# Kernel optimization log

Hardware: AMD Instinct MI355X
Metric: run time of the kernel (lower is better)

Reference implementation:

```python
import jax, jax.numpy as jnp
import numpy as np
import math

B, S, D, K = 8, 2048, 1024, 64
EPS = 1e-5

def _ln(x):
    m = jnp.mean(x, axis=-1, keepdims=True)
    v = jnp.mean((x - m) ** 2, axis=-1, keepdims=True)
    return (x - m) * jax.lax.rsqrt(v + EPS)

def setup_inputs() -> dict:
    key = jax.random.key(0)
    ks = jax.random.split(key, 14)
    s = 0.02
    return {
        "x":  jax.random.normal(ks[0], (B, S, D), dtype=jnp.float32),
        "Wk": jax.random.normal(ks[1], (D, K), dtype=jnp.float32) * s,
        "bk": jnp.zeros((K,), dtype=jnp.float32),
        "Wq": jax.random.normal(ks[2], (D, K), dtype=jnp.float32) * s,
        "bq": jnp.zeros((K,), dtype=jnp.float32),
        "Wv": jax.random.normal(ks[3], (D, D), dtype=jnp.float32) * s,
        "bv": jnp.zeros((D,), dtype=jnp.float32),
        "Wb": jax.random.normal(ks[4], (D, 1), dtype=jnp.float32) * s,
        "bb": jnp.zeros((1,), dtype=jnp.float32),
        "W1": jax.random.normal(ks[5], (D, D), dtype=jnp.float32) * s,
        "b1": jnp.zeros((D,), dtype=jnp.float32),
        "g1": jnp.ones((D,), dtype=jnp.float32),
        "be1": jnp.zeros((D,), dtype=jnp.float32),
    }

def reference(x, Wk, bk, Wq, bq, Wv, bv, Wb, bb, W1, b1, g1, be1):
    scale = 1.0 / math.sqrt(K)
    keys    = (jnp.einsum('bsd,dk->bsk', x, Wk) + bk) * scale   # [B,S,K]
    queries = jnp.einsum('bsd,dk->bsk', x, Wq) + bq             # [B,S,K]
    values  = jnp.einsum('bsd,de->bse', x, Wv) + bv             # [B,S,D]
    biases  = jnp.einsum('bsd,do->bso', x, Wb) + bb             # [B,S,1]
    # scores[b,i,j] = keys[b,i] . queries[b,j] + biases[b,i]
    scores = jax.nn.sigmoid(jnp.einsum('bik,bjk->bij', keys, queries) + biases)
    attention = jnp.einsum('bij,bjd->bid', scores, values)      # [B,S,D]
    res = _ln(x + attention) * g1 + be1
    feedforward = jax.nn.relu(jnp.einsum('bsd,de->bse', res, W1) + b1)
    return _ln(res + feedforward)
```

## Files before the change

### kernel.cpp

```cpp
#include <hip/hip_runtime.h>
#include <math.h>


typedef __bf16 bf16_t;
typedef __bf16 bf16x4_t __attribute__((ext_vector_type(4)));
typedef __bf16 bf16x8_t __attribute__((ext_vector_type(8)));
typedef float  f32x4    __attribute__((ext_vector_type(4)));

#define DEV static __device__ __forceinline__

DEV void gll16(const void* g, void* l) {
  __builtin_amdgcn_global_load_lds(
      (const __attribute__((address_space(1))) void*)g,
      (__attribute__((address_space(3))) void*)l, 16, 0, 0);
}

__global__ __launch_bounds__(512, 4) void vt_kq(
    const bf16_t* __restrict__ Wvt, const bf16_t* __restrict__ x_bf,
    bf16_t* __restrict__ vt, const float* __restrict__ bv,
    const bf16_t* __restrict__ Wkqt, bf16_t* __restrict__ kqO,
    const float* __restrict__ bk, const float* __restrict__ bq) {
  __shared__ bf16_t SM[24576];
  const int tid = threadIdx.x;
  const int wid = tid >> 6, l = tid & 63;
  const int lr = l & 15, lh = l >> 4;
  const int sw = (lh ^ ((lr >> 1) & 3)) * 8;

  if (blockIdx.x < 512) {
#define ASH(s) (&SM[(s) << 13])
#define BSH(s) (&SM[16384 + ((s) << 12)])
    const int nwg = 512;
    const int orig = blockIdx.x;
    const int lid = (orig & 7) * (nwg >> 3) + (orig >> 3);
    const int bx = lid / 4;
    const int by = lid % 4;
    const int m0 = by * 256, n0 = bx * 128;
    const int lda = 1024, ldb = 1024, ldc = 16384;

    const int wr = wid >> 1, wc = wid & 1;
    const int sRow = tid >> 2;
    const int sSl = (tid & 3) ^ ((tid >> 3) & 3);
    const bf16_t* Asrc = Wvt + (long)(m0 + sRow) * lda + sSl * 8;
    const bf16_t* Bsrc = x_bf + (long)(n0 + sRow) * ldb + sSl * 8;
    const long aStep = (long)128 * lda;

    const int aOff = (wr * 64 + lr) * 32 + sw;
    const int bOff = (wc * 64 + lr) * 32 + sw;

    f32x4 acc[4][4] = {};

    gll16(Asrc, ASH(0) + tid * 8);
    gll16(Asrc + aStep, ASH(0) + 4096 + tid * 8);
    gll16(Bsrc, BSH(0) + tid * 8);

    for (int h = 0; h < 32; ++h) {
      const int s = h & 1;
      asm volatile("s_waitcnt vmcnt(0)" ::: "memory");
      __builtin_amdgcn_sched_barrier(0);
      __builtin_amdgcn_s_barrier();
      if (h + 1 < 32) {
        const bf16_t* a_ = Asrc + (h + 1) * 32;
        const bf16_t* b_ = Bsrc + (h + 1) * 32;
        gll16(a_, ASH(s ^ 1) + tid * 8);
        gll16(a_ + aStep, ASH(s ^ 1) + 4096 + tid * 8);
        gll16(b_, BSH(s ^ 1) + tid * 8);
      }
      bf16x8_t aF[4], bF[4];
#pragma unroll
      for (int m = 0; m < 4; ++m) aF[m] = *(const bf16x8_t*)(ASH(s) + aOff + m * 512);
#pragma unroll
      for (int n = 0; n < 4; ++n) bF[n] = *(const bf16x8_t*)(BSH(s) + bOff + n * 512);
      asm volatile("s_waitcnt lgkmcnt(0)" ::: "memory");
      __builtin_amdgcn_sched_barrier(0);
      __builtin_amdgcn_s_setprio(1);
#pragma unroll
      for (int m = 0; m < 4; ++m)
#pragma unroll
        for (int n = 0; n < 4; ++n)
          acc[m][n] = __builtin_amdgcn_mfma_f32_16x16x32_bf16(aF[m], bF[n], acc[m][n], 0, 0, 0);
      __builtin_amdgcn_s_setprio(0);
    }

    const int rowb = m0 + wr * 64 + lh * 4;
    const int colb = n0 + wc * 64 + lr;
#pragma unroll
    for (int m = 0; m < 4; ++m)
#pragma unroll
      for (int n = 0; n < 4; ++n) {
        const f32x4 v = acc[m][n];
        const int cc = colb + n * 16;
#pragma unroll
        for (int r = 0; r < 4; ++r) {
          const int rr = rowb + m * 16 + r;
          vt[(long)rr * ldc + cc] = (bf16_t)(v[r] + bv[rr]);
        }
      }
#undef ASH
#undef BSH
  } else {
#define ASH(s) (&SM[(s) << 12])
#define BSH(s) (&SM[8192 + ((s) << 12)])
    const int m0 = (blockIdx.x - 512) * 128;

    const int sRow = tid >> 2;
    const int sSl = (tid & 3) ^ ((tid >> 3) & 3);
    const bf16_t* Asrc = x_bf + (long)(m0 + sRow) * 1024 + sSl * 8;
    const bf16_t* Bsrc = Wkqt + (long)sRow * 1024 + sSl * 8;

    const int aOff = (wid * 16 + lr) * 32 + sw;

    f32x4 acc[8] = {};

    gll16(Asrc, ASH(0) + tid * 8);
    gll16(Bsrc, BSH(0) + tid * 8);

    for (int h = 0; h < 32; ++h) {
      const int s = h & 1;
      asm volatile("s_waitcnt vmcnt(0)" ::: "memory");
      __builtin_amdgcn_sched_barrier(0);
      __builtin_amdgcn_s_barrier();
      if (h + 1 < 32) {
        gll16(Asrc + (h + 1) * 32, ASH(s ^ 1) + tid * 8);
        gll16(Bsrc + (h + 1) * 32, BSH(s ^ 1) + tid * 8);
      }
      const bf16x8_t aF = *(const bf16x8_t*)(ASH(s) + aOff);
      bf16x8_t bF[8];
#pragma unroll
      for (int j = 0; j < 8; ++j)
        bF[j] = *(const bf16x8_t*)(BSH(s) + (j * 16 + lr) * 32 + sw);
      asm volatile("s_waitcnt lgkmcnt(0)" ::: "memory");
      __builtin_amdgcn_sched_barrier(0);
      __builtin_amdgcn_s_setprio(1);
#pragma unroll
      for (int j = 0; j < 8; ++j)
        acc[j] = __builtin_amdgcn_mfma_f32_16x16x32_bf16(aF, bF[j], acc[j], 0, 0, 0);
      __builtin_amdgcn_s_setprio(0);
    }

    __builtin_amdgcn_s_barrier();
#pragma unroll
    for (int j = 0; j < 8; ++j) {
      const f32x4 v = acc[j];
      const int cl = j * 16 + lr;
      const float b = (cl < 64) ? bk[cl] : bq[cl - 64];
      const float sc = (cl < 64) ? 0.125f : 1.0f;
#pragma unroll
      for (int r = 0; r < 4; ++r) {
        const int rl = wid * 16 + lh * 4 + r;
        SM[rl * 128 + (cl ^ (lh << 4))] = (bf16_t)((v[r] + b) * sc);
      }
    }
    __builtin_amdgcn_s_barrier();
    const int chunk = tid & 15, rsub = tid >> 4;
#pragma unroll
    for (int pp = 0; pp < 4; ++pp) {
      const int rl = pp * 32 + rsub;
      const int sc = chunk ^ (((rl >> 2) & 3) << 1);
      const bf16x8_t vv = *(const bf16x8_t*)&SM[rl * 128 + sc * 8];
      *(bf16x8_t*)&kqO[(long)(m0 + rl) * 128 + chunk * 8] = vv;
    }
#undef ASH
#undef BSH
  }
}

template <int MODE, int MFAST>
__global__ __launch_bounds__(512, 4) void gemm128n(
    const bf16_t* __restrict__ A, const bf16_t* __restrict__ B,
    bf16_t* __restrict__ C, int K, int lda, int ldb, int ldc,
    const float* __restrict__ aux0) {
  const int gx = gridDim.x, gy = gridDim.y;
  const int nwg = gx * gy;
  const int orig = blockIdx.x + gx * blockIdx.y;
  const int lid = (orig & 7) * (nwg >> 3) + (orig >> 3);
  const int bx = MFAST ? (lid / gy) : (lid % gx);
  const int by = MFAST ? (lid % gy) : (lid / gx);
  const int m0 = by * 256, n0 = bx * 128;

  __shared__ bf16_t SM[24576];
#define ASH(s) (&SM[(s) << 13])
#define BSH(s) (&SM[16384 + ((s) << 12)])

  const int tid = threadIdx.x;
  const int wid = tid >> 6, l = tid & 63;
  const int wr = wid >> 1, wc = wid & 1;
  const int lr = l & 15, lh = l >> 4;

  const int sRow = tid >> 2;
  const int sSl = (tid & 3) ^ ((tid >> 3) & 3);
  const bf16_t* Asrc = A + (long)(m0 + sRow) * lda + sSl * 8;
  const bf16_t* Bsrc = B + (long)(n0 + sRow) * ldb + sSl * 8;
  const long aStep = (long)128 * lda;

  const int sw = (lh ^ ((lr >> 1) & 3)) * 8;
  const int aOff = (wr * 64 + lr) * 32 + sw;
  const int bOff = (wc * 64 + lr) * 32 + sw;

  f32x4 acc[4][4] = {};
  const int NT = K >> 5;

  gll16(Asrc, ASH(0) + tid * 8);
  gll16(Asrc + aStep, ASH(0) + 4096 + tid * 8);
  gll16(Bsrc, BSH(0) + tid * 8);

  for (int h = 0; h < NT; ++h) {
    const int s = h & 1;
    asm volatile("s_waitcnt vmcnt(0)" ::: "memory");
    __builtin_amdgcn_sched_barrier(0);
    __builtin_amdgcn_s_barrier();
    if (h + 1 < NT) {
      const bf16_t* a_ = Asrc + (h + 1) * 32;
      const bf16_t* b_ = Bsrc + (h + 1) * 32;
      gll16(a_, ASH(s ^ 1) + tid * 8);
      gll16(a_ + aStep, ASH(s ^ 1) + 4096 + tid * 8);
      gll16(b_, BSH(s ^ 1) + tid * 8);
    }
    bf16x8_t aF[4], bF[4];
#pragma unroll
    for (int m = 0; m < 4; ++m) aF[m] = *(const bf16x8_t*)(ASH(s) + aOff + m * 512);
#pragma unroll
    for (int n = 0; n < 4; ++n) bF[n] = *(const bf16x8_t*)(BSH(s) + bOff + n * 512);
    asm volatile("s_waitcnt lgkmcnt(0)" ::: "memory");
    __builtin_amdgcn_sched_barrier(0);
    __builtin_amdgcn_s_setprio(1);
#pragma unroll
    for (int m = 0; m < 4; ++m)
#pragma unroll
      for (int n = 0; n < 4; ++n)
        acc[m][n] = __builtin_amdgcn_mfma_f32_16x16x32_bf16(aF[m], bF[n], acc[m][n], 0, 0, 0);
    __builtin_amdgcn_s_setprio(0);
  }

  const int rowb = m0 + wr * 64 + lh * 4;
  const int colb = n0 + wc * 64 + lr;
#pragma unroll
  for (int m = 0; m < 4; ++m)
#pragma unroll
    for (int n = 0; n < 4; ++n) {
      const f32x4 v = acc[m][n];
      const int cc = colb + n * 16;
#pragma unroll
      for (int r = 0; r < 4; ++r) {
        const int rr = rowb + m * 16 + r;
        const float val = v[r];
        if constexpr (MODE == 1) {
          C[(long)rr * ldc + cc] = (bf16_t)(val + aux0[rr]);
        } else {
          C[(long)rr * ldc + cc] = (bf16_t)fmaxf(val + aux0[cc], 0.0f);
        }
      }
    }
#undef ASH
#undef BSH
}

template <int MODE>
__global__ __launch_bounds__(512, 2) void gemm256p(
    const bf16_t* __restrict__ A, const bf16_t* __restrict__ B,
    bf16_t* __restrict__ C, int K, int lda, int ldb, int ldc,
    long sAb, long sBb, long sCb, const float* __restrict__ aux0) {
  const int gx = gridDim.x, gy = gridDim.y;
  const int gxy = gx * gy;
  const int nwg = gxy * (int)gridDim.z;
  const int orig = blockIdx.x + gx * blockIdx.y + gxy * blockIdx.z;
  const int lid = (orig & 7) * (nwg >> 3) + (orig >> 3);
  const int bz = lid / gxy;
  const int rem = lid - bz * gxy;
  const int bx = rem % gx;
  const int by = rem / gx;

  A += (long)bz * sAb;
  B += (long)bz * sBb;
  const int m0 = by * 256, n0 = bx * 256;

  __shared__ bf16_t SM[65536];
#define ASH(b, h) (&SM[(((b)*2 + (h)) << 13)])
#define BSH(b, h) (&SM[32768 + (((b)*2 + (h)) << 13)])

  const int tid = threadIdx.x;
  const int wid = tid >> 6, l = tid & 63;
  const int wr = wid >> 2, wc = wid & 3;
  const int lr = l & 15, lh = l >> 4;

  const int sRow = tid >> 2;
  const int sSl = (tid & 3) ^ ((tid >> 3) & 3);
  const bf16_t* Asrc = A + (long)(m0 + sRow) * lda + sSl * 8;
  const bf16_t* Bsrc = B + (long)(n0 + sRow) * ldb + sSl * 8;
  const long aStep = (long)128 * lda, bStep = (long)128 * ldb;

#define STAGE_A(b, h, kt) do { \
    const bf16_t* s_ = Asrc + (kt) * 64 + (h) * 32; \
    gll16(s_,         ASH(b, h) + tid * 8); \
    gll16(s_ + aStep, ASH(b, h) + 4096 + tid * 8); } while (0)
#define STAGE_B(b, h, kt) do { \
    const bf16_t* s_ = Bsrc + (kt) * 64 + (h) * 32; \
    gll16(s_,         BSH(b, h) + tid * 8); \
    gll16(s_ + bStep, BSH(b, h) + 4096 + tid * 8); } while (0)

  const int sw = (lh ^ ((lr >> 1) & 3)) * 8;
  const int aOff = (wr * 128 + lr) * 32 + sw;
  const int bOff = (wc * 64 + lr) * 32 + sw;

  f32x4 acc[8][4] = {};
  const int NT = K >> 6;

#define LGKM(n) do { \
    asm volatile("s_waitcnt lgkmcnt(" #n ")" ::: "memory"); \
    __builtin_amdgcn_sched_barrier(0); } while (0)
#define MFMA16(AS, BS, mo) do { \
    __builtin_amdgcn_s_setprio(1); \
    _Pragma("unroll") for (int m = 0; m < 4; ++m) \
    _Pragma("unroll") for (int n = 0; n < 4; ++n) \
      acc[m + (mo)][n] = __builtin_amdgcn_mfma_f32_16x16x32_bf16(AS[m], BS[n], acc[m + (mo)][n], 0, 0, 0); \
    __builtin_amdgcn_s_setprio(0); } while (0)

  STAGE_A(0, 0, 0); STAGE_B(0, 0, 0); STAGE_A(0, 1, 0); STAGE_B(0, 1, 0);
  asm volatile("s_waitcnt vmcnt(4)" ::: "memory");
  __builtin_amdgcn_s_barrier();

  bf16x8_t aA[4], aB[4], bA[4], bB[4];
#pragma unroll
  for (int n = 0; n < 4; ++n) bA[n] = *(const bf16x8_t*)(BSH(0, 0) + bOff + n * 512);
#pragma unroll
  for (int m = 0; m < 4; ++m) aA[m] = *(const bf16x8_t*)(ASH(0, 0) + aOff + m * 512);

  for (int t = 0; t < NT; ++t) {
    const int p = t & 1, q = p ^ 1;
    const bool pf = (t + 1 < NT);

#pragma unroll
    for (int m = 0; m < 4; ++m) aB[m] = *(const bf16x8_t*)(ASH(p, 0) + aOff + (m + 4) * 512);
    if (pf) STAGE_A(q, 0, t + 1);
    LGKM(4);
    MFMA16(aA, bA, 0);

    if (pf) {
      asm volatile("s_waitcnt vmcnt(2)" ::: "memory");
    } else {
      asm volatile("s_waitcnt vmcnt(0)" ::: "memory");
    }
    __builtin_amdgcn_sched_barrier(0);
    __builtin_amdgcn_s_barrier();
#pragma unroll
    for (int m = 0; m < 4; ++m) aA[m] = *(const bf16x8_t*)(ASH(p, 1) + aOff + m * 512);
#pragma unroll
    for (int n = 0; n < 4; ++n) bB[n] = *(const bf16x8_t*)(BSH(p, 1) + bOff + n * 512);
    if (pf) STAGE_B(q, 0, t + 1);
    LGKM(8);
    MFMA16(aB, bA, 4);

#pragma unroll
    for (int m = 0; m < 4; ++m) aB[m] = *(const bf16x8_t*)(ASH(p, 1) + aOff + (m + 4) * 512);
    if (pf) STAGE_A(q, 1, t + 1);
    LGKM(4);
    MFMA16(aA, bB, 0);

    if (pf) STAGE_B(q, 1, t + 1);
    asm volatile("s_waitcnt lgkmcnt(0)" ::: "memory");
    if (pf) {
      asm volatile("s_waitcnt vmcnt(4)" ::: "memory");
    }
    __builtin_amdgcn_sched_barrier(0);
    __builtin_amdgcn_s_barrier();
    if (pf) {
#pragma unroll
      for (int n = 0; n < 4; ++n) bA[n] = *(const bf16x8_t*)(BSH(q, 0) + bOff + n * 512);
#pragma unroll
      for (int m = 0; m < 4; ++m) aA[m] = *(const bf16x8_t*)(ASH(q, 0) + aOff + m * 512);
    }
    __builtin_amdgcn_sched_barrier(0);
    MFMA16(aB, bB, 4);
  }
#undef STAGE_A
#undef STAGE_B
#undef LGKM
#undef MFMA16

  bf16_t* Cb = C + (long)bz * sCb;
  const int rowb = m0 + wr * 128 + lh * 4;
  const int colb = n0 + wc * 64 + lr;
#pragma unroll
  for (int m = 0; m < 8; ++m)
#pragma unroll
    for (int n = 0; n < 4; ++n) {
      const f32x4 v = acc[m][n];
      const int cc = colb + n * 16;
#pragma unroll
      for (int r = 0; r < 4; ++r) {
        const int rr = rowb + m * 16 + r;
        Cb[(long)rr * ldc + cc] = (bf16_t)v[r];
      }
    }
#undef ASH
#undef BSH
}

__global__ __launch_bounds__(256) void scores128(
    const bf16_t* __restrict__ kq, bf16_t* __restrict__ C,
    const float* __restrict__ biases) {
  const int orig = blockIdx.x + 16 * blockIdx.y + 256 * blockIdx.z;
  const int lid = (orig & 7) * 256 + (orig >> 3);
  const int bz = lid >> 8;
  const int rem = lid & 255;
  const int bx = rem & 15, by = rem >> 4;

  const bf16_t* A = kq + (long)bz * 2048 * 128;
  const bf16_t* B = A + 64;
  const float* a0 = biases + (long)bz * 2048;
  const int m0 = by * 128, n0 = bx * 128;

  __shared__ bf16_t SM[16384];
#define ASH(h) (&SM[(h) << 12])
#define BSH(h) (&SM[8192 + ((h) << 12)])

  const int tid = threadIdx.x;
  const int w = tid >> 6, l = tid & 63;
  const int wr = w >> 1, wc = w & 1;
  const int lr = l & 15, lh = l >> 4;

  const int sRow = tid >> 2;
  const int sSl = ((tid & 3) ^ ((tid >> 3) & 3)) * 8;
  const bf16_t* As = A + (long)(m0 + sRow) * 128 + sSl;
  const bf16_t* Bs = B + (long)(n0 + sRow) * 128 + sSl;
#pragma unroll
  for (int h = 0; h < 2; ++h) {
    gll16(As + h * 32, ASH(h) + tid * 8);
    gll16(As + h * 32 + 64 * 128, ASH(h) + 2048 + tid * 8);
    gll16(Bs + h * 32, BSH(h) + tid * 8);
    gll16(Bs + h * 32 + 64 * 128, BSH(h) + 2048 + tid * 8);
  }
  asm volatile("s_waitcnt vmcnt(0)" ::: "memory");
  __builtin_amdgcn_s_barrier();

  const int sw = (lh ^ ((lr >> 1) & 3)) * 8;
  const int aOff = (wr * 64 + lr) * 32 + sw;
  const int bOff = (wc * 64 + lr) * 32 + sw;

  f32x4 acc[4][4] = {};
#pragma unroll
  for (int h = 0; h < 2; ++h) {
    bf16x8_t aF[4], bF[4];
#pragma unroll
    for (int m = 0; m < 4; ++m) aF[m] = *(const bf16x8_t*)(ASH(h) + aOff + m * 512);
#pragma unroll
    for (int n = 0; n < 4; ++n) bF[n] = *(const bf16x8_t*)(BSH(h) + bOff + n * 512);
#pragma unroll
    for (int m = 0; m < 4; ++m)
#pragma unroll
      for (int n = 0; n < 4; ++n)
        acc[m][n] = __builtin_amdgcn_mfma_f32_16x16x32_bf16(aF[m], bF[n], acc[m][n], 0, 0, 0);
  }

  __builtin_amdgcn_s_barrier();
  {
    const int rowb = (wr << 6) + (lh << 2);
    const int colb = (wc << 6) + lr;
#pragma unroll
    for (int m = 0; m < 4; ++m)
#pragma unroll
      for (int n = 0; n < 4; ++n) {
        const f32x4 v = acc[m][n];
        const int cl = colb + (n << 4);
#pragma unroll
        for (int r = 0; r < 4; ++r) {
          const int rl = rowb + (m << 4) + r;
          const float zz = v[r] + a0[m0 + rl];
          SM[rl * 128 + (cl ^ (lh << 4))] =
              (bf16_t)__builtin_amdgcn_rcpf(1.0f + __expf(-zz));
        }
      }
    __syncthreads();
    bf16_t* Cb = C + (long)bz * 2048 * 2048;
    const int chunk = tid & 15, rsub = tid >> 4;
#pragma unroll
    for (int pp = 0; pp < 8; ++pp) {
      const int rl = pp * 16 + rsub;
      const int sc = chunk ^ (((rl >> 2) & 3) << 1);
      const bf16x8_t vv = *(const bf16x8_t*)&SM[rl * 128 + sc * 8];
      *(bf16x8_t*)&Cb[(long)(m0 + rl) * 2048 + n0 + chunk * 8] = vv;
    }
  }
#undef ASH
#undef BSH
}

__global__ __launch_bounds__(256) void prep(
    const float* __restrict__ x, const float* __restrict__ Wb,
    const float* __restrict__ bb, bf16_t* __restrict__ x_bf,
    float* __restrict__ biases,
    const float* __restrict__ Wk, const float* __restrict__ Wq,
    const float* __restrict__ Wv, const float* __restrict__ W1,
    bf16_t* __restrict__ Wkqt, bf16_t* __restrict__ Wvt,
    bf16_t* __restrict__ W1t) {
  __shared__ float t[32][33];
  if (blockIdx.x < 4096) {
    const int r = blockIdx.x * 4 + (threadIdx.x >> 6);
    const int l = threadIdx.x & 63;
    const float* xr = x + (long)r * 1024;
    bf16_t* orow = x_bf + (long)r * 1024;
    float s = 0.f;
#pragma unroll
    for (int i = 0; i < 4; ++i) {
      const int off = l * 4 + i * 256;
      const float4 v = *(const float4*)(xr + off);
      const float4 w = *(const float4*)(Wb + off);
      s += v.x * w.x + v.y * w.y + v.z * w.z + v.w * w.w;
      bf16x4_t o;
      o[0] = (bf16_t)v.x; o[1] = (bf16_t)v.y; o[2] = (bf16_t)v.z; o[3] = (bf16_t)v.w;
      *(bf16x4_t*)(orow + off) = o;
    }
#pragma unroll
    for (int off = 1; off < 64; off <<= 1) s += __shfl_xor(s, off);
    if (l == 0) biases[r] = s + bb[0];
    return;
  }
  int b = blockIdx.x - 4096;
  const float* in;
  bf16_t* out;
  int R = 1024, C, c0, r0;
  if (b < 1024) {
    in = Wv; out = Wvt; C = 1024;
    c0 = (b & 31) * 32; r0 = (b >> 5) * 32;
  } else if (b < 2048) {
    b -= 1024; in = W1; out = W1t; C = 1024;
    c0 = (b & 31) * 32; r0 = (b >> 5) * 32;
  } else if (b < 2112) {
    b -= 2048; in = Wk; out = Wkqt; C = 64;
    c0 = (b & 1) * 32; r0 = (b >> 1) * 32;
  } else {
    b -= 2112; in = Wq; out = Wkqt + 64 * 1024; C = 64;
    c0 = (b & 1) * 32; r0 = (b >> 1) * 32;
  }
  const int tx = threadIdx.x & 31, ty = threadIdx.x >> 5;
#pragma unroll
  for (int i = 0; i < 4; ++i) {
    const int rl = ty * 4 + i;
    t[rl][tx] = in[(long)(r0 + rl) * C + c0 + tx];
  }
  __syncthreads();
#pragma unroll
  for (int i = 0; i < 4; ++i) {
    const int rl = ty * 4 + i;
    out[(long)(c0 + rl) * R + r0 + tx] = (bf16_t)t[tx][rl];
  }
}

__global__ __launch_bounds__(256) void ln1_kernel(
    const bf16_t* __restrict__ x, const bf16_t* __restrict__ attn,
    const float* __restrict__ g, const float* __restrict__ be,
    bf16_t* __restrict__ res) {
  const int w = threadIdx.x >> 6, l = threadIdx.x & 63;
  const long r = (long)blockIdx.x * 4 + w;
  const bf16_t* xr = x + r * 1024;
  const bf16_t* ar = attn + r * 1024;
  float y[16];
  float s = 0.f, ss = 0.f;
#pragma unroll
  for (int h = 0; h < 2; ++h) {
    const int base = h * 512 + l * 8;
    const bf16x8_t xv = *(const bf16x8_t*)(xr + base);
    const bf16x8_t av = *(const bf16x8_t*)(ar + base);
#pragma unroll
    for (int j = 0; j < 8; ++j) {
      const float yy = (float)xv[j] + (float)av[j];
      y[h * 8 + j] = yy;
      s += yy; ss += yy * yy;
    }
  }
#pragma unroll
  for (int off = 1; off < 64; off <<= 1) {
    s += __shfl_xor(s, off);
    ss += __shfl_xor(ss, off);
  }
  const float mean = s * (1.0f / 1024.0f);
  const float rs = rsqrtf(ss * (1.0f / 1024.0f) - mean * mean + 1e-5f);
  bf16_t* orow = res + r * 1024;
#pragma unroll
  for (int h = 0; h < 2; ++h) {
    const int base = h * 512 + l * 8;
    bf16x8_t o;
#pragma unroll
    for (int j = 0; j < 8; ++j)
      o[j] = (bf16_t)((y[h * 8 + j] - mean) * rs * g[base + j] + be[base + j]);
    *(bf16x8_t*)(orow + base) = o;
  }
}

__global__ __launch_bounds__(256) void ln2_kernel(
    const bf16_t* __restrict__ res, const bf16_t* __restrict__ hh,
    float* __restrict__ out) {
  const int w = threadIdx.x >> 6, l = threadIdx.x & 63;
  const long r = (long)blockIdx.x * 4 + w;
  const bf16_t* rr = res + r * 1024;
  const bf16_t* hr = hh + r * 1024;
  float y[16];
  float s = 0.f, ss = 0.f;
#pragma unroll
  for (int h = 0; h < 2; ++h) {
    const int base = h * 512 + l * 8;
    const bf16x8_t rv = *(const bf16x8_t*)(rr + base);
    const bf16x8_t hv = *(const bf16x8_t*)(hr + base);
#pragma unroll
    for (int j = 0; j < 8; ++j) {
      const float yy = (float)rv[j] + (float)hv[j];
      y[h * 8 + j] = yy;
      s += yy; ss += yy * yy;
    }
  }
#pragma unroll
  for (int off = 1; off < 64; off <<= 1) {
    s += __shfl_xor(s, off);
    ss += __shfl_xor(ss, off);
  }
  const float mean = s * (1.0f / 1024.0f);
  const float rs = rsqrtf(ss * (1.0f / 1024.0f) - mean * mean + 1e-5f);
  float* orow = out + r * 1024;
#pragma unroll
  for (int h = 0; h < 2; ++h) {
    const int base = h * 512 + l * 8;
    float4 o1, o2;
    o1.x = (y[h * 8 + 0] - mean) * rs; o1.y = (y[h * 8 + 1] - mean) * rs;
    o1.z = (y[h * 8 + 2] - mean) * rs; o1.w = (y[h * 8 + 3] - mean) * rs;
    o2.x = (y[h * 8 + 4] - mean) * rs; o2.y = (y[h * 8 + 5] - mean) * rs;
    o2.z = (y[h * 8 + 6] - mean) * rs; o2.w = (y[h * 8 + 7] - mean) * rs;
    *(float4*)(orow + base) = o1;
    *(float4*)(orow + base + 4) = o2;
  }
}

extern "C" void kernel_launch(void* const* d_in, const int* in_sizes, int n_in,
                              void* d_out, int out_size, void* d_ws, size_t ws_size,
                              hipStream_t stream) {
  const float* x   = (const float*)d_in[0];
  const float* Wk  = (const float*)d_in[1];
  const float* bk  = (const float*)d_in[2];
  const float* Wq  = (const float*)d_in[3];
  const float* bq  = (const float*)d_in[4];
  const float* Wv  = (const float*)d_in[5];
  const float* bv  = (const float*)d_in[6];
  const float* Wb  = (const float*)d_in[7];
  const float* bb  = (const float*)d_in[8];
  const float* W1  = (const float*)d_in[9];
  const float* b1  = (const float*)d_in[10];
  const float* g1  = (const float*)d_in[11];
  const float* be1 = (const float*)d_in[12];
  float* out = (float*)d_out;

  char* ws = (char*)d_ws;
  bf16_t* x_bf    = (bf16_t*)(ws + 0);
  bf16_t* vt_bf   = (bf16_t*)(ws + 33554432);
  bf16_t* kq_bf   = (bf16_t*)(ws + 67108864);
  bf16_t* Wkqt    = (bf16_t*)(ws + 71303168);
  bf16_t* Wvt     = (bf16_t*)(ws + 71565312);
  bf16_t* W1t     = (bf16_t*)(ws + 73662464);
  float*  biases  = (float*) (ws + 75759616);
  bf16_t* scores  = (bf16_t*)(ws + 75825152);
  bf16_t* attn_bf = (bf16_t*)(ws + 142934016);
  bf16_t* res_bf  = (bf16_t*)(ws + 176488448);
  bf16_t* h_bf    = attn_bf;

  prep<<<6272, 256, 0, stream>>>(x, Wb, bb, x_bf, biases,
                                 Wk, Wq, Wv, W1, Wkqt, Wvt, W1t);

  vt_kq<<<640, 512, 0, stream>>>(Wvt, x_bf, vt_bf, bv, Wkqt, kq_bf, bk, bq);

  scores128<<<dim3(16, 16, 8), 256, 0, stream>>>(kq_bf, scores, biases);

  gemm256p<3><<<dim3(4, 8, 8), 512, 0, stream>>>(
      scores, vt_bf, attn_bf, 2048, 2048, 16384, 1024,
      2048L * 2048, 2048, 2048L * 1024, nullptr);

  ln1_kernel<<<4096, 256, 0, stream>>>(x_bf, attn_bf, g1, be1, res_bf);

  gemm128n<4, 0><<<dim3(8, 64), 512, 0, stream>>>(
      res_bf, W1t, h_bf, 1024, 1024, 1024, 1024, b1);

  ln2_kernel<<<4096, 256, 0, stream>>>(res_bf, h_bf, out);
}
```

Baseline: 231.0 us.

## Replace 256x256 attention-value GEMM with 256x128 tile kernel at higher occupancy

Replaces the heavily hand-pipelined 256x256-tile gemm256p for scores·V with a new gemm128a using 256x128 tiles, 48 KB LDS, and a simple double-buffered K=32 loop. This doubles the grid to 512 blocks and raises occupancy (launch bounds 4 instead of 2), aiming to fill the GPU better and hide latency through more resident waves. In exchange it gives up the finer-grained intra-iteration overlap and lowers data reuse per tile, and it adds a full barrier plus vmcnt(0) wait every 32-wide K step.

```diff
diff --git a/kernel.cpp b/kernel.cpp
--- a/kernel.cpp
+++ b/kernel.cpp
@@ -13,6 +13,93 @@
   __builtin_amdgcn_global_load_lds(
       (const __attribute__((address_space(1))) void*)g,
       (__attribute__((address_space(3))) void*)l, 16, 0, 0);
+}
+
+__global__ __launch_bounds__(512, 4) void gemm128a(
+    const bf16_t* __restrict__ scores, const bf16_t* __restrict__ vt,
+    bf16_t* __restrict__ attn) {
+  const int nwg = 512;
+  const int orig = blockIdx.x;
+  const int lid = (orig & 7) * (nwg >> 3) + (orig >> 3);
+  const int bz = lid >> 6;
+  const int rem = lid & 63;
+  const int bx = rem & 7;
+  const int by = rem >> 3;
+  const int m0 = by * 256, n0 = bx * 128;
+
+  const bf16_t* A = scores + (long)bz * 2048 * 2048;
+  const bf16_t* B = vt + (long)bz * 2048;
+  bf16_t* C = attn + (long)bz * 2048 * 1024;
+
+  __shared__ bf16_t SM[24576];
+#define ASH(s) (&SM[(s) << 13])
+#define BSH(s) (&SM[16384 + ((s) << 12)])
+
+  const int tid = threadIdx.x;
+  const int wid = tid >> 6, l = tid & 63;
+  const int wr = wid >> 1, wc = wid & 1;
+  const int lr = l & 15, lh = l >> 4;
+
+  const int sRow = tid >> 2;
+  const int sSl = (tid & 3) ^ ((tid >> 3) & 3);
+  const bf16_t* Asrc = A + (long)(m0 + sRow) * 2048 + sSl * 8;
+  const bf16_t* Bsrc = B + (long)(n0 + sRow) * 16384 + sSl * 8;
+  const long aStep = (long)128 * 2048;
+
+  const int sw = (lh ^ ((lr >> 1) & 3)) * 8;
+  const int aOff = (wr * 64 + lr) * 32 + sw;
+  const int bOff = (wc * 64 + lr) * 32 + sw;
+
+  f32x4 acc[4][4] = {};
+
+  gll16(Asrc, ASH(0) + tid * 8);
+  gll16(Asrc + aStep, ASH(0) + 4096 + tid * 8);
+  gll16(Bsrc, BSH(0) + tid * 8);
+
+  for (int h = 0; h < 64; ++h) {
+    const int s = h & 1;
+    asm volatile("s_waitcnt vmcnt(0)" ::: "memory");
+    __builtin_amdgcn_sched_barrier(0);
+    __builtin_amdgcn_s_barrier();
+    if (h + 1 < 64) {
+      const bf16_t* a_ = Asrc + (h + 1) * 32;
+      const bf16_t* b_ = Bsrc + (h + 1) * 32;
+      gll16(a_, ASH(s ^ 1) + tid * 8);
+      gll16(a_ + aStep, ASH(s ^ 1) + 4096 + tid * 8);
+      gll16(b_, BSH(s ^ 1) + tid * 8);
+    }
+    bf16x8_t aF[4], bF[4];
+#pragma unroll
+    for (int m = 0; m < 4; ++m) aF[m] = *(const bf16x8_t*)(ASH(s) + aOff + m * 512);
+#pragma unroll
+    for (int n = 0; n < 4; ++n) bF[n] = *(const bf16x8_t*)(BSH(s) + bOff + n * 512);
+    asm volatile("s_waitcnt lgkmcnt(0)" ::: "memory");
+    __builtin_amdgcn_sched_barrier(0);
+    __builtin_amdgcn_s_setprio(1);
+#pragma unroll
+    for (int m = 0; m < 4; ++m)
+#pragma unroll
+      for (int n = 0; n < 4; ++n)
+        acc[m][n] = __builtin_amdgcn_mfma_f32_16x16x32_bf16(aF[m], bF[n], acc[m][n], 0, 0, 0);
+    __builtin_amdgcn_s_setprio(0);
+  }
+
+  const int rowb = m0 + wr * 64 + lh * 4;
+  const int colb = n0 + wc * 64 + lr;
+#pragma unroll
+  for (int m = 0; m < 4; ++m)
+#pragma unroll
+    for (int n = 0; n < 4; ++n) {
+      const f32x4 v = acc[m][n];
+      const int cc = colb + n * 16;
+#pragma unroll
+      for (int r = 0; r < 4; ++r) {
+        const int rr = rowb + m * 16 + r;
+        C[(long)rr * 1024 + cc] = (bf16_t)v[r];
+      }
+    }
+#undef ASH
+#undef BSH
 }
 
 __global__ __launch_bounds__(512, 4) void vt_kq(
@@ -248,147 +335,6 @@
         } else {
           C[(long)rr * ldc + cc] = (bf16_t)fmaxf(val + aux0[cc], 0.0f);
         }
-      }
-    }
-#undef ASH
-#undef BSH
-}
-
-template <int MODE>
-__global__ __launch_bounds__(512, 2) void gemm256p(
-    const bf16_t* __restrict__ A, const bf16_t* __restrict__ B,
-    bf16_t* __restrict__ C, int K, int lda, int ldb, int ldc,
-    long sAb, long sBb, long sCb, const float* __restrict__ aux0) {
-  const int gx = gridDim.x, gy = gridDim.y;
-  const int gxy = gx * gy;
-  const int nwg = gxy * (int)gridDim.z;
-  const int orig = blockIdx.x + gx * blockIdx.y + gxy * blockIdx.z;
-  const int lid = (orig & 7) * (nwg >> 3) + (orig >> 3);
-  const int bz = lid / gxy;
-  const int rem = lid - bz * gxy;
-  const int bx = rem % gx;
-  const int by = rem / gx;
-
-  A += (long)bz * sAb;
-  B += (long)bz * sBb;
-  const int m0 = by * 256, n0 = bx * 256;
-
-  __shared__ bf16_t SM[65536];
-#define ASH(b, h) (&SM[(((b)*2 + (h)) << 13)])
-#define BSH(b, h) (&SM[32768 + (((b)*2 + (h)) << 13)])
-
-  const int tid = threadIdx.x;
-  const int wid = tid >> 6, l = tid & 63;
-  const int wr = wid >> 2, wc = wid & 3;
-  const int lr = l & 15, lh = l >> 4;
-
-  const int sRow = tid >> 2;
-  const int sSl = (tid & 3) ^ ((tid >> 3) & 3);
-  const bf16_t* Asrc = A + (long)(m0 + sRow) * lda + sSl * 8;
-  const bf16_t* Bsrc = B + (long)(n0 + sRow) * ldb + sSl * 8;
-  const long aStep = (long)128 * lda, bStep = (long)128 * ldb;
-
-#define STAGE_A(b, h, kt) do { \
-    const bf16_t* s_ = Asrc + (kt) * 64 + (h) * 32; \
-    gll16(s_,         ASH(b, h) + tid * 8); \
-    gll16(s_ + aStep, ASH(b, h) + 4096 + tid * 8); } while (0)
-#define STAGE_B(b, h, kt) do { \
-    const bf16_t* s_ = Bsrc + (kt) * 64 + (h) * 32; \
-    gll16(s_,         BSH(b, h) + tid * 8); \
-    gll16(s_ + bStep, BSH(b, h) + 4096 + tid * 8); } while (0)
-
-  const int sw = (lh ^ ((lr >> 1) & 3)) * 8;
-  const int aOff = (wr * 128 + lr) * 32 + sw;
-  const int bOff = (wc * 64 + lr) * 32 + sw;
-
-  f32x4 acc[8][4] = {};
-  const int NT = K >> 6;
-
-#define LGKM(n) do { \
-    asm volatile("s_waitcnt lgkmcnt(" #n ")" ::: "memory"); \
-    __builtin_amdgcn_sched_barrier(0); } while (0)
-#define MFMA16(AS, BS, mo) do { \
-    __builtin_amdgcn_s_setprio(1); \
-    _Pragma("unroll") for (int m = 0; m < 4; ++m) \
-    _Pragma("unroll") for (int n = 0; n < 4; ++n) \
-      acc[m + (mo)][n] = __builtin_amdgcn_mfma_f32_16x16x32_bf16(AS[m], BS[n], acc[m + (mo)][n], 0, 0, 0); \
-    __builtin_amdgcn_s_setprio(0); } while (0)
-
-  STAGE_A(0, 0, 0); STAGE_B(0, 0, 0); STAGE_A(0, 1, 0); STAGE_B(0, 1, 0);
-  asm volatile("s_waitcnt vmcnt(4)" ::: "memory");
-  __builtin_amdgcn_s_barrier();
-
-  bf16x8_t aA[4], aB[4], bA[4], bB[4];
-#pragma unroll
-  for (int n = 0; n < 4; ++n) bA[n] = *(const bf16x8_t*)(BSH(0, 0) + bOff + n * 512);
-#pragma unroll
-  for (int m = 0; m < 4; ++m) aA[m] = *(const bf16x8_t*)(ASH(0, 0) + aOff + m * 512);
-
-  for (int t = 0; t < NT; ++t) {
-    const int p = t & 1, q = p ^ 1;
-    const bool pf = (t + 1 < NT);
-
-#pragma unroll
-    for (int m = 0; m < 4; ++m) aB[m] = *(const bf16x8_t*)(ASH(p, 0) + aOff + (m + 4) * 512);
-    if (pf) STAGE_A(q, 0, t + 1);
-    LGKM(4);
-    MFMA16(aA, bA, 0);
-
-    if (pf) {
-      asm volatile("s_waitcnt vmcnt(2)" ::: "memory");
-    } else {
-      asm volatile("s_waitcnt vmcnt(0)" ::: "memory");
-    }
-    __builtin_amdgcn_sched_barrier(0);
-    __builtin_amdgcn_s_barrier();
-#pragma unroll
-    for (int m = 0; m < 4; ++m) aA[m] = *(const bf16x8_t*)(ASH(p, 1) + aOff + m * 512);
-#pragma unroll
-    for (int n = 0; n < 4; ++n) bB[n] = *(const bf16x8_t*)(BSH(p, 1) + bOff + n * 512);
-    if (pf) STAGE_B(q, 0, t + 1);
-    LGKM(8);
-    MFMA16(aB, bA, 4);
-
-#pragma unroll
-    for (int m = 0; m < 4; ++m) aB[m] = *(const bf16x8_t*)(ASH(p, 1) + aOff + (m + 4) * 512);
-    if (pf) STAGE_A(q, 1, t + 1);
-    LGKM(4);
-    MFMA16(aA, bB, 0);
-
-    if (pf) STAGE_B(q, 1, t + 1);
-    asm volatile("s_waitcnt lgkmcnt(0)" ::: "memory");
-    if (pf) {
-      asm volatile("s_waitcnt vmcnt(4)" ::: "memory");
-    }
-    __builtin_amdgcn_sched_barrier(0);
-    __builtin_amdgcn_s_barrier();
-    if (pf) {
-#pragma unroll
-      for (int n = 0; n < 4; ++n) bA[n] = *(const bf16x8_t*)(BSH(q, 0) + bOff + n * 512);
-#pragma unroll
-      for (int m = 0; m < 4; ++m) aA[m] = *(const bf16x8_t*)(ASH(q, 0) + aOff + m * 512);
-    }
-    __builtin_amdgcn_sched_barrier(0);
-    MFMA16(aB, bB, 4);
-  }
-#undef STAGE_A
-#undef STAGE_B
-#undef LGKM
-#undef MFMA16
-
-  bf16_t* Cb = C + (long)bz * sCb;
-  const int rowb = m0 + wr * 128 + lh * 4;
-  const int colb = n0 + wc * 64 + lr;
-#pragma unroll
-  for (int m = 0; m < 8; ++m)
-#pragma unroll
-    for (int n = 0; n < 4; ++n) {
-      const f32x4 v = acc[m][n];
-      const int cc = colb + n * 16;
-#pragma unroll
-      for (int r = 0; r < 4; ++r) {
-        const int rr = rowb + m * 16 + r;
-        Cb[(long)rr * ldc + cc] = (bf16_t)v[r];
       }
     }
 #undef ASH
@@ -666,9 +612,7 @@
 
   scores128<<<dim3(16, 16, 8), 256, 0, stream>>>(kq_bf, scores, biases);
 
-  gemm256p<3><<<dim3(4, 8, 8), 512, 0, stream>>>(
-      scores, vt_bf, attn_bf, 2048, 2048, 16384, 1024,
-      2048L * 2048, 2048, 2048L * 1024, nullptr);
+  gemm128a<<<512, 512, 0, stream>>>(scores, vt_bf, attn_bf);
 
   ln1_kernel<<<4096, 256, 0, stream>>>(x_bf, attn_bf, g1, be1, res_bf);
 
```

New measurement: 235.9 us. +2.1%, slower.
